# Kernel tuning notes

Measured on AMD Instinct MI355X. Metric: run time of the kernel, lower is better.

Reference implementation:

```python
import jax, jax.numpy as jnp
import numpy as np

N, L, HOP = 512, 16, 8  # L // 2


def overlap_and_add(frames, hop):
    # frames: [..., K, L] -> [..., (K-1)*hop + L]
    K, Lf = frames.shape[-2], frames.shape[-1]
    T = (K - 1) * hop + Lf
    idx = (jnp.arange(K)[:, None] * hop + jnp.arange(Lf)[None, :]).reshape(-1)
    flat = frames.reshape(frames.shape[:-2] + (K * Lf,))
    out = jnp.zeros(frames.shape[:-2] + (T,), frames.dtype)
    return out.at[..., idx].add(flat)


def setup_inputs() -> dict:
    key = jax.random.key(0)
    k1, k2, k3 = jax.random.split(key, 3)
    M, C, K = 8, 2, 6000
    inputs = jax.random.normal(k1, (M, N, K), dtype=jnp.float32)
    est_mask = jax.random.uniform(k2, (M, C, N, K), dtype=jnp.float32)
    W = jax.random.normal(k3, (N, L), dtype=jnp.float32) * 0.05
    return {"inputs": inputs, "est_mask": est_mask, "W": W}


def reference(inputs, est_mask, W):
    # masked source spectra: [M, C, N, K]
    masked = inputs[:, None, :, :] * est_mask
    # transpose to [M, C, K, N] and project N -> L (fused in einsum)
    frames = jnp.einsum('mcnk,nl->mckl', masked, W)  # [M, C, K, L]
    # overlap-and-add with hop L // 2 -> [M, C, T]
    return overlap_and_add(frames, HOP)
```

## Files before the change

kernel.cpp:

```cpp
#include <hip/hip_runtime.h>

#define NN   512
#define LL   16
#define MM   8
#define CC   2
#define KK   6000
#define TT   ((KK - 1) * 8 + 16)
#define KW   128
#define NKB  47
#define NKBP 48
#define NCH  16
#define NC   (NN / NCH)
#define ROWB (KK * 4)
#define TENS_B (NCH * KW * 4)
#define BUF_B  (3 * TENS_B)

typedef __attribute__((address_space(3))) void       lds_v;
typedef __attribute__((address_space(1))) const void glob_v;

__global__ __launch_bounds__(512, 4) void decoder_dma_kernel(
    const float* __restrict__ inputs,
    const float* __restrict__ est_mask,
    const float* __restrict__ W,
    float* __restrict__ out)
{
    __shared__ __align__(16) char lds[2 * BUF_B];

    const int bid = blockIdx.x;
    const int xcd = bid & 7;
    const int s   = bid >> 3;
    const int kb  = xcd * 6 + (s % 6);
    const int m   = s / 6;
    if (kb >= NKB) return;

    const int tid = threadIdx.x;
    const int t   = tid & 63;
    const int wq  = __builtin_amdgcn_readfirstlane(tid >> 6);

    const int lane_r = t >> 5;
    int cb = kb * 512 + (t & 31) * 16;
    if (cb > ROWB - 16) cb = ROWB - 16;
    const size_t lane_off = (size_t)lane_r * ROWB + cb;

    const char* tb0 = (const char*)inputs   + (size_t)m * NN * ROWB;
    const char* tb1 = (const char*)est_mask + (size_t)(m * CC) * NN * ROWB;
    const char* tb2 = tb1 + (size_t)NN * ROWB;

    char* dst_base = lds + wq * 1024;

    auto issue = [&](int c, int bsel) {
        const size_t rowoff = (size_t)(c * NCH + wq * 2) * ROWB + lane_off;
        char* bb = dst_base + bsel * BUF_B;
        __builtin_amdgcn_global_load_lds((glob_v*)(tb0 + rowoff), (lds_v*)(bb),              16, 0, 0);
        __builtin_amdgcn_global_load_lds((glob_v*)(tb1 + rowoff), (lds_v*)(bb + TENS_B),     16, 0, 0);
        __builtin_amdgcn_global_load_lds((glob_v*)(tb2 + rowoff), (lds_v*)(bb + 2 * TENS_B), 16, 0, 0);
    };

    float a0A[LL], a0B[LL], a1A[LL], a1B[LL];
    #pragma unroll
    for (int l = 0; l < LL; ++l) { a0A[l] = 0.f; a0B[l] = 0.f; a1A[l] = 0.f; a1B[l] = 0.f; }

    issue(0, 0);

    for (int c = 0; c < NC; ++c) {
        if (c + 1 < NC) {
            issue(c + 1, (c + 1) & 1);
            asm volatile("s_waitcnt vmcnt(3)" ::: "memory");
        } else {
            asm volatile("s_waitcnt vmcnt(0)" ::: "memory");
        }
        __builtin_amdgcn_sched_barrier(0);

        const char* Lb = lds + (c & 1) * BUF_B + wq * 1024;

        #pragma unroll
        for (int r = 0; r < 2; ++r) {
            const int n = c * NCH + wq * 2 + r;
            float wv[LL];
            *reinterpret_cast<float4*>(&wv[0])  = *(const float4*)(W + n * LL + 0);
            *reinterpret_cast<float4*>(&wv[4])  = *(const float4*)(W + n * LL + 4);
            *reinterpret_cast<float4*>(&wv[8])  = *(const float4*)(W + n * LL + 8);
            *reinterpret_cast<float4*>(&wv[12]) = *(const float4*)(W + n * LL + 12);

            const float2 vin = reinterpret_cast<const float2*>(Lb + r * 512)[t];
            const float2 vm0 = reinterpret_cast<const float2*>(Lb + TENS_B + r * 512)[t];
            const float2 vm1 = reinterpret_cast<const float2*>(Lb + 2 * TENS_B + r * 512)[t];
            const float x0A = vin.x * vm0.x, x0B = vin.y * vm0.y;
            const float x1A = vin.x * vm1.x, x1B = vin.y * vm1.y;
            #pragma unroll
            for (int l = 0; l < LL; ++l) {
                a0A[l] = fmaf(x0A, wv[l], a0A[l]);
                a0B[l] = fmaf(x0B, wv[l], a0B[l]);
                a1A[l] = fmaf(x1A, wv[l], a1A[l]);
                a1B[l] = fmaf(x1B, wv[l], a1B[l]);
            }
        }
    }

    __syncthreads();

    float* sm = (float*)lds;
    if (wq >= 4) {
        float* d = &sm[((wq - 4) * 64 + t) * 33];
        #pragma unroll
        for (int l = 0; l < LL; ++l) { d[l] = a0A[l]; d[16 + l] = a0B[l]; }
    }
    __syncthreads();
    if (wq < 4) {
        const float* sp = &sm[(wq * 64 + t) * 33];
        #pragma unroll
        for (int l = 0; l < LL; ++l) { a0A[l] += sp[l]; a0B[l] += sp[16 + l]; }
    }
    __syncthreads();
    if (wq >= 4) {
        float* d = &sm[((wq - 4) * 64 + t) * 33];
        #pragma unroll
        for (int l = 0; l < LL; ++l) { d[l] = a1A[l]; d[16 + l] = a1B[l]; }
    }
    __syncthreads();
    if (wq < 4) {
        const float* sp = &sm[(wq * 64 + t) * 33];
        #pragma unroll
        for (int l = 0; l < LL; ++l) { a1A[l] += sp[l]; a1B[l] += sp[16 + l]; }
    }
    __syncthreads();
    if (wq == 2 || wq == 3) {
        float* d = &sm[((wq - 2) * 64 + t) * 67];
        #pragma unroll
        for (int l = 0; l < LL; ++l) {
            d[l] = a0A[l]; d[16 + l] = a0B[l];
            d[32 + l] = a1A[l]; d[48 + l] = a1B[l];
        }
    }
    __syncthreads();
    if (wq < 2) {
        const float* sp = &sm[(wq * 64 + t) * 67];
        #pragma unroll
        for (int l = 0; l < LL; ++l) {
            a0A[l] += sp[l]; a0B[l] += sp[16 + l];
            a1A[l] += sp[32 + l]; a1B[l] += sp[48 + l];
        }
    }
    __syncthreads();
    if (wq == 1) {
        float* d = &sm[t * 67];
        #pragma unroll
        for (int l = 0; l < LL; ++l) {
            d[l] = a0A[l]; d[16 + l] = a0B[l];
            d[32 + l] = a1A[l]; d[48 + l] = a1B[l];
        }
    }
    __syncthreads();

    if (wq == 0) {
        {
            const float* sp = &sm[t * 67];
            #pragma unroll
            for (int l = 0; l < LL; ++l) {
                a0A[l] += sp[l]; a0B[l] += sp[16 + l];
                a1A[l] += sp[32 + l]; a1B[l] += sp[48 + l];
            }
        }

        const int kA = kb * KW + 2 * t;
        float ph0[8], ph1[8];
        #pragma unroll
        for (int j = 0; j < 8; ++j) {
            ph0[j] = __shfl_up(a0B[8 + j], 1);
            ph1[j] = __shfl_up(a1B[8 + j], 1);
        }

        if (kA < KK) {
            float* o0 = out + ((size_t)m * CC + 0) * TT + 8 * kA;
            float* o1 = out + ((size_t)m * CC + 1) * TT + 8 * kA;

            if (t == 0) {
                #pragma unroll
                for (int j = 0; j < 8; ++j) {
                    atomicAdd(&o0[j], a0A[j]);
                    atomicAdd(&o1[j], a1A[j]);
                }
            } else {
                #pragma unroll
                for (int j = 0; j < 8; ++j) {
                    o0[j] = a0A[j] + ph0[j];
                    o1[j] = a1A[j] + ph1[j];
                }
            }
            #pragma unroll
            for (int j = 0; j < 8; ++j) {
                o0[8 + j] = a0B[j] + a0A[8 + j];
                o1[8 + j] = a1B[j] + a1A[8 + j];
            }
            const int kB = kA + 1;
            if (t == 63 || kB == KK - 1) {
                #pragma unroll
                for (int j = 0; j < 8; ++j) {
                    atomicAdd(&o0[16 + j], a0B[8 + j]);
                    atomicAdd(&o1[16 + j], a1B[8 + j]);
                }
            }
        }
    }
}

extern "C" void kernel_launch(void* const* d_in, const int* in_sizes, int n_in,
                              void* d_out, int out_size, void* d_ws, size_t ws_size,
                              hipStream_t stream) {
    const float* inputs   = (const float*)d_in[0];
    const float* est_mask = (const float*)d_in[1];
    const float* W        = (const float*)d_in[2];
    float*       out      = (float*)d_out;

    hipMemsetAsync(out, 0, (size_t)out_size * sizeof(float), stream);

    decoder_dma_kernel<<<dim3(NKBP * MM), 512, 0, stream>>>(inputs, est_mask, W, out);
}
```

Before: 58.94 us.

## Widen K tile to 256 with block-shared row chunks and two-deep prefetch

Doubles the K-width per block to 256 columns, which halves the grid to 192 blocks. Each wave now DMAs one full contiguous 1 KB row segment into LDS, and pairs of waves share the rows for compute. Loads are issued two chunks ahead, with block barriers guarding buffer reuse. The cross-wave reduction shrinks from 8 to 4 groups, which cuts LDS reduction passes and edge atomics. In exchange, a 192-block grid leaves many of the MI355X's compute units idle for a bandwidth-bound kernel, and two s_barriers are added per chunk.

```diff
diff --git a/kernel.cpp b/kernel.cpp
--- a/kernel.cpp
+++ b/kernel.cpp
@@ -6,13 +6,12 @@
 #define CC   2
 #define KK   6000
 #define TT   ((KK - 1) * 8 + 16)
-#define KW   128
-#define NKB  47
-#define NKBP 48
-#define NCH  16
-#define NC   (NN / NCH)
+#define KW   256
+#define NKB  24
+#define CHR  8
+#define NC   (NN / CHR)
 #define ROWB (KK * 4)
-#define TENS_B (NCH * KW * 4)
+#define TENS_B (CHR * 1024)
 #define BUF_B  (3 * TENS_B)
 
 typedef __attribute__((address_space(3))) void       lds_v;
@@ -29,31 +28,28 @@
     const int bid = blockIdx.x;
     const int xcd = bid & 7;
     const int s   = bid >> 3;
-    const int kb  = xcd * 6 + (s % 6);
-    const int m   = s / 6;
-    if (kb >= NKB) return;
+    const int kb  = xcd * 3 + (s % 3);
+    const int m   = s / 3;
 
     const int tid = threadIdx.x;
     const int t   = tid & 63;
     const int wq  = __builtin_amdgcn_readfirstlane(tid >> 6);
-
-    const int lane_r = t >> 5;
-    int cb = kb * 512 + (t & 31) * 16;
+    const int g   = wq >> 1;
+    const int p   = (wq & 1) * 64 + t;
+
+    int cb = kb * 1024 + t * 16;
     if (cb > ROWB - 16) cb = ROWB - 16;
-    const size_t lane_off = (size_t)lane_r * ROWB + cb;
 
     const char* tb0 = (const char*)inputs   + (size_t)m * NN * ROWB;
     const char* tb1 = (const char*)est_mask + (size_t)(m * CC) * NN * ROWB;
     const char* tb2 = tb1 + (size_t)NN * ROWB;
 
-    char* dst_base = lds + wq * 1024;
-
     auto issue = [&](int c, int bsel) {
-        const size_t rowoff = (size_t)(c * NCH + wq * 2) * ROWB + lane_off;
-        char* bb = dst_base + bsel * BUF_B;
-        __builtin_amdgcn_global_load_lds((glob_v*)(tb0 + rowoff), (lds_v*)(bb),              16, 0, 0);
-        __builtin_amdgcn_global_load_lds((glob_v*)(tb1 + rowoff), (lds_v*)(bb + TENS_B),     16, 0, 0);
-        __builtin_amdgcn_global_load_lds((glob_v*)(tb2 + rowoff), (lds_v*)(bb + 2 * TENS_B), 16, 0, 0);
+        const size_t off = (size_t)(c * CHR + wq) * ROWB + cb;
+        char* bb = lds + bsel * BUF_B + wq * 1024;
+        __builtin_amdgcn_global_load_lds((glob_v*)(tb0 + off), (lds_v*)(bb),              16, 0, 0);
+        __builtin_amdgcn_global_load_lds((glob_v*)(tb1 + off), (lds_v*)(bb + TENS_B),     16, 0, 0);
+        __builtin_amdgcn_global_load_lds((glob_v*)(tb2 + off), (lds_v*)(bb + 2 * TENS_B), 16, 0, 0);
     };
 
     float a0A[LL], a0B[LL], a1A[LL], a1B[LL];
@@ -61,30 +57,33 @@
     for (int l = 0; l < LL; ++l) { a0A[l] = 0.f; a0B[l] = 0.f; a1A[l] = 0.f; a1B[l] = 0.f; }
 
     issue(0, 0);
+    issue(1, 1);
 
     for (int c = 0; c < NC; ++c) {
         if (c + 1 < NC) {
-            issue(c + 1, (c + 1) & 1);
             asm volatile("s_waitcnt vmcnt(3)" ::: "memory");
         } else {
             asm volatile("s_waitcnt vmcnt(0)" ::: "memory");
         }
         __builtin_amdgcn_sched_barrier(0);
-
-        const char* Lb = lds + (c & 1) * BUF_B + wq * 1024;
-
-        #pragma unroll
-        for (int r = 0; r < 2; ++r) {
-            const int n = c * NCH + wq * 2 + r;
+        __builtin_amdgcn_s_barrier();
+        __builtin_amdgcn_sched_barrier(0);
+
+        const char* Lb = lds + (c & 1) * BUF_B;
+
+        #pragma unroll
+        for (int rloc = 0; rloc < 2; ++rloc) {
+            const int lr = 2 * g + rloc;
+            const int n  = c * CHR + lr;
             float wv[LL];
             *reinterpret_cast<float4*>(&wv[0])  = *(const float4*)(W + n * LL + 0);
             *reinterpret_cast<float4*>(&wv[4])  = *(const float4*)(W + n * LL + 4);
             *reinterpret_cast<float4*>(&wv[8])  = *(const float4*)(W + n * LL + 8);
             *reinterpret_cast<float4*>(&wv[12]) = *(const float4*)(W + n * LL + 12);
 
-            const float2 vin = reinterpret_cast<const float2*>(Lb + r * 512)[t];
-            const float2 vm0 = reinterpret_cast<const float2*>(Lb + TENS_B + r * 512)[t];
-            const float2 vm1 = reinterpret_cast<const float2*>(Lb + 2 * TENS_B + r * 512)[t];
+            const float2 vin = *reinterpret_cast<const float2*>(Lb + lr * 1024 + p * 8);
+            const float2 vm0 = *reinterpret_cast<const float2*>(Lb + TENS_B + lr * 1024 + p * 8);
+            const float2 vm1 = *reinterpret_cast<const float2*>(Lb + 2 * TENS_B + lr * 1024 + p * 8);
             const float x0A = vin.x * vm0.x, x0B = vin.y * vm0.y;
             const float x1A = vin.x * vm1.x, x1B = vin.y * vm1.y;
             #pragma unroll
@@ -95,37 +94,42 @@
                 a1B[l] = fmaf(x1B, wv[l], a1B[l]);
             }
         }
+
+        __builtin_amdgcn_sched_barrier(0);
+        __builtin_amdgcn_s_barrier();
+        __builtin_amdgcn_sched_barrier(0);
+        if (c + 2 < NC) issue(c + 2, c & 1);
     }
 
     __syncthreads();
 
     float* sm = (float*)lds;
-    if (wq >= 4) {
-        float* d = &sm[((wq - 4) * 64 + t) * 33];
+    if (g >= 2) {
+        float* d = &sm[((g - 2) * 128 + p) * 33];
         #pragma unroll
         for (int l = 0; l < LL; ++l) { d[l] = a0A[l]; d[16 + l] = a0B[l]; }
     }
     __syncthreads();
-    if (wq < 4) {
-        const float* sp = &sm[(wq * 64 + t) * 33];
+    if (g < 2) {
+        const float* sp = &sm[(g * 128 + p) * 33];
         #pragma unroll
         for (int l = 0; l < LL; ++l) { a0A[l] += sp[l]; a0B[l] += sp[16 + l]; }
     }
     __syncthreads();
-    if (wq >= 4) {
-        float* d = &sm[((wq - 4) * 64 + t) * 33];
+    if (g >= 2) {
+        float* d = &sm[((g - 2) * 128 + p) * 33];
         #pragma unroll
         for (int l = 0; l < LL; ++l) { d[l] = a1A[l]; d[16 + l] = a1B[l]; }
     }
     __syncthreads();
-    if (wq < 4) {
-        const float* sp = &sm[(wq * 64 + t) * 33];
+    if (g < 2) {
+        const float* sp = &sm[(g * 128 + p) * 33];
         #pragma unroll
         for (int l = 0; l < LL; ++l) { a1A[l] += sp[l]; a1B[l] += sp[16 + l]; }
     }
     __syncthreads();
-    if (wq == 2 || wq == 3) {
-        float* d = &sm[((wq - 2) * 64 + t) * 67];
+    if (g == 1) {
+        float* d = &sm[p * 67];
         #pragma unroll
         for (int l = 0; l < LL; ++l) {
             d[l] = a0A[l]; d[16 + l] = a0B[l];
@@ -133,28 +137,10 @@
         }
     }
     __syncthreads();
-    if (wq < 2) {
-        const float* sp = &sm[(wq * 64 + t) * 67];
-        #pragma unroll
-        for (int l = 0; l < LL; ++l) {
-            a0A[l] += sp[l]; a0B[l] += sp[16 + l];
-            a1A[l] += sp[32 + l]; a1B[l] += sp[48 + l];
-        }
-    }
-    __syncthreads();
-    if (wq == 1) {
-        float* d = &sm[t * 67];
-        #pragma unroll
-        for (int l = 0; l < LL; ++l) {
-            d[l] = a0A[l]; d[16 + l] = a0B[l];
-            d[32 + l] = a1A[l]; d[48 + l] = a1B[l];
-        }
-    }
-    __syncthreads();
-
-    if (wq == 0) {
+
+    if (g == 0) {
         {
-            const float* sp = &sm[t * 67];
+            const float* sp = &sm[p * 67];
             #pragma unroll
             for (int l = 0; l < LL; ++l) {
                 a0A[l] += sp[l]; a0B[l] += sp[16 + l];
@@ -162,7 +148,7 @@
             }
         }
 
-        const int kA = kb * KW + 2 * t;
+        const int kA = kb * KW + 2 * p;
         float ph0[8], ph1[8];
         #pragma unroll
         for (int j = 0; j < 8; ++j) {
@@ -214,5 +200,5 @@
 
     hipMemsetAsync(out, 0, (size_t)out_size * sizeof(float), stream);
 
-    decoder_dma_kernel<<<dim3(NKBP * MM), 512, 0, stream>>>(inputs, est_mask, W, out);
+    decoder_dma_kernel<<<dim3(NKB * MM), 512, 0, stream>>>(inputs, est_mask, W, out);
 }
```

New measurement: 83.38 us. 1.41x slower.
